# Performance work log

Measured on AMD Instinct MI355X. Metric: run time of the kernel, lower is better.

## Reference

```python
import jax, jax.numpy as jnp
import numpy as np

T, B, H, L = 2048, 32, 512, 2  # seq_len, batch, hidden(=input), num_layers
G = 4 * H
W_SCALE = 0.05  # keep randn-initialized weights out of deep gate saturation


def setup_inputs() -> dict:
    key = jax.random.key(0)
    ks = jax.random.split(key, 5)
    return {
        "x": jax.random.normal(ks[0], (T, B, H), dtype=jnp.float32),
        "w_ih": jax.random.normal(ks[1], (L, G, H), dtype=jnp.float32) * W_SCALE,
        "w_hh": jax.random.normal(ks[2], (L, G, H), dtype=jnp.float32) * W_SCALE,
        "b_ih": jax.random.normal(ks[3], (L, G), dtype=jnp.float32) * W_SCALE,
        "b_hh": jax.random.normal(ks[4], (L, G), dtype=jnp.float32) * W_SCALE,
        "h0": jnp.zeros((L, B, H), dtype=jnp.float32),
        "c0": jnp.zeros((L, B, H), dtype=jnp.float32),
    }


def _lstm_layer(x, w_ih, w_hh, b_ih, b_hh, h0, c0):
    # Precompute input-side gate contributions for all timesteps at once:
    # gates_x[t] = x[t] @ w_ih.T + b_ih + b_hh   (shape [T, B, 4H])
    gates_x = jnp.einsum("tbi,gi->tbg", x, w_ih) + b_ih + b_hh

    def step(carry, gx):
        h, c = carry
        gates = gx + h @ w_hh.T  # [B, 4H]
        i, f, g, o = jnp.split(gates, 4, axis=-1)  # chunk(4, 1) order: i,f,g,o
        i = jax.nn.sigmoid(i)
        f = jax.nn.sigmoid(f)
        g = jnp.tanh(g)
        o = jax.nn.sigmoid(o)
        c = f * c + i * g
        h = o * jnp.tanh(c)
        return (h, c), h

    (hT, cT), ys = jax.lax.scan(step, (h0, c0), gates_x)
    return ys, hT, cT


def reference(x, w_ih, w_hh, b_ih, b_hh, h0, c0):
    out = x
    h_fin, c_fin = [], []
    for l in range(L):  # small fixed stack of structurally identical layers
        out, hT, cT = _lstm_layer(out, w_ih[l], w_hh[l], b_ih[l], b_hh[l], h0[l], c0[l])
        h_fin.append(hT)
        c_fin.append(cT)
    return out, jnp.stack(h_fin), jnp.stack(c_fin)
```

## Files before the change

### kernel.cpp

```cpp
#include <hip/hip_runtime.h>
#include <hip/hip_bf16.h>
#include <stdint.h>

#define T_LEN 2048
#define BATCH 32
#define HID   512
#define GDIM  2048
#define NL    2
#define NBL   32
#define UPB   16
#define RSL   16
#define BH    (BATCH*HID)
#define SLOTB (BH*2)
#define RINGB (RSL*SLOTB)

#define FZ_FB   2048
#define FZ_DET  4096
#define FZ_ABT  4160
#define FZ_TOT  4224

typedef __attribute__((ext_vector_type(8))) __bf16         bf16x8;
typedef __attribute__((ext_vector_type(8))) unsigned short u16x8;
typedef __attribute__((ext_vector_type(4))) unsigned short u16x4;
typedef __attribute__((ext_vector_type(4))) float          f32x4;

__device__ __forceinline__ unsigned short f2bf(float f) {
  unsigned int u = __builtin_bit_cast(unsigned int, f);
  u += 0x7FFFu + ((u >> 16) & 1u);
  return (unsigned short)(u >> 16);
}
__device__ __forceinline__ f32x4 pack8(f32x4 a, f32x4 b) {
  u16x8 r;
  r[0]=f2bf(a[0]); r[1]=f2bf(a[1]); r[2]=f2bf(a[2]); r[3]=f2bf(a[3]);
  r[4]=f2bf(b[0]); r[5]=f2bf(b[1]); r[6]=f2bf(b[2]); r[7]=f2bf(b[3]);
  return __builtin_bit_cast(f32x4, r);
}
__device__ __forceinline__ float sigm(float x)  { return 1.0f / (1.0f + __expf(-x)); }
__device__ __forceinline__ float tanh_(float x) { return 2.0f / (1.0f + __expf(-2.0f*x)) - 1.0f; }

__device__ __forceinline__ f32x4 ld16_pl(const void* p)  { f32x4 r; asm volatile("global_load_dwordx4 %0, %1, off"     : "=v"(r) : "v"(p)); return r; }
__device__ __forceinline__ f32x4 ld16_sc0(const void* p) { f32x4 r; asm volatile("global_load_dwordx4 %0, %1, off sc0" : "=v"(r) : "v"(p)); return r; }
__device__ __forceinline__ f32x4 ld16_sc1(const void* p) { f32x4 r; asm volatile("global_load_dwordx4 %0, %1, off sc1" : "=v"(r) : "v"(p)); return r; }
__device__ __forceinline__ int lddww_sc1(const void* p) {
  int r; asm volatile("global_load_dword %0, %1, off sc1\n\ts_waitcnt vmcnt(0)" : "=v"(r) : "v"(p) : "memory"); return r;
}
__device__ __forceinline__ void st2_sc0(void* p, unsigned short v) {
  unsigned int vv = v; asm volatile("global_store_short %0, %1, off sc0" :: "v"(p), "v"(vv) : "memory");
}
__device__ __forceinline__ void st2_sc1(void* p, unsigned short v) {
  unsigned int vv = v; asm volatile("global_store_short %0, %1, off sc1" :: "v"(p), "v"(vv) : "memory");
}
__device__ __forceinline__ void stdw_sc1(void* p, int v) { asm volatile("global_store_dword %0, %1, off sc1" :: "v"(p), "v"(v) : "memory"); }
__device__ __forceinline__ void vm_drain() { asm volatile("s_waitcnt vmcnt(0)" ::: "memory"); }


__global__ void prep_misc(const float* __restrict__ b_ih, const float* __restrict__ b_hh,
                          const float* __restrict__ h0,
                          int* __restrict__ flagz, float* __restrict__ bsum,
                          char* __restrict__ ring0, char* __restrict__ ring1s) {
  int i = blockIdx.x * blockDim.x + threadIdx.x;
  if (i < FZ_TOT) flagz[i] = 0;
  if (i < NL*GDIM) bsum[i] = b_ih[i] + b_hh[i];
  if (i < NL*2048) {
    int layer = i >> 11, id = i & 2047;
    int mh = id >> 10, ks = (id >> 6) & 15, lf = id & 63;
    int c2 = lf & 15, k2 = lf >> 4;
    const float* s = h0 + ((size_t)(layer*BATCH + mh*16 + c2))*HID + ks*32 + k2*8;
    f32x4 v = pack8(*(const f32x4*)s, *(const f32x4*)(s+4));
    *(f32x4*)(ring0  + (size_t)layer*RINGB + (size_t)id*16) = v;
    *(f32x4*)(ring1s + (size_t)layer*RINGB + (size_t)id*16) = v;
  }
}

__global__ void prep_w(const float* __restrict__ wih, const float* __restrict__ whh,
                       unsigned short* __restrict__ wihb, unsigned short* __restrict__ whhb) {
  const int n4 = NL*GDIM*HID/4;
  for (int i = blockIdx.x*blockDim.x + threadIdx.x; i < 2*n4; i += gridDim.x*blockDim.x) {
    const float*    src = (i < n4) ? wih  : whh;
    unsigned short* dst = (i < n4) ? wihb : whhb;
    int j = (i < n4) ? i : i - n4;
    f32x4 v = *((const f32x4*)src + j);
    u16x4 o; o[0]=f2bf(v[0]); o[1]=f2bf(v[1]); o[2]=f2bf(v[2]); o[3]=f2bf(v[3]);
    *((u16x4*)dst + j) = o;
  }
}


__global__ __launch_bounds__(512, 2) void lstm_persist(
    const float* __restrict__ x, const float* __restrict__ c0,
    const unsigned short* __restrict__ wihb, const unsigned short* __restrict__ whhb,
    const float* __restrict__ bsum,
    char* __restrict__ ring0, char* __restrict__ ring1s,
    int* __restrict__ flagz, float* __restrict__ out) {

  const int bid = blockIdx.x;
  const int r8  = bid & 7;
  if (r8 >= NL) return;
  const int layer = r8;
  const int lb    = bid >> 3;
  const int actIdx = layer*NBL + lb;
  const int tid  = threadIdx.x;
  const int lane = tid & 63;
  const int wave = tid >> 6;
  const int mh = wave & 1, nh = wave >> 1;
  const int col = lane & 15, kg = lane >> 4;
  const int gt  = col & 3;
  const int uu  = nh*4 + (col >> 2);
  const int u0  = lb * UPB;
  const int gu  = u0 + uu;
  const int grow = gt*HID + gu;
  const int tb  = mh*16 + kg*4 + gt;

  int* flagsA = flagz;
  int* flagsB = flagz + FZ_FB;
  int* detect = flagz + FZ_DET;
  int* abortp = flagz + FZ_ABT;

  __shared__ __align__(16) f32x4 smem[4096];

  f32x4 wfx[16], wfh[16];
  {
    const unsigned short* wxr = wihb + ((size_t)(layer*GDIM + grow))*HID + kg*8;
    const unsigned short* whr = whhb + ((size_t)(layer*GDIM + grow))*HID + kg*8;
#pragma unroll
    for (int ks = 0; ks < 16; ++ks) {
      wfx[ks] = *(const f32x4*)(wxr + ks*32);
      wfh[ks] = *(const f32x4*)(whr + ks*32);
    }
  }

  float c = c0[((size_t)layer*BATCH + tb)*HID + gu];
  const float bi  = bsum[layer*GDIM + 0*HID + gu];
  const float bfv = bsum[layer*GDIM + 1*HID + gu];
  const float bg  = bsum[layer*GDIM + 2*HID + gu];
  const float bo  = bsum[layer*GDIM + 3*HID + gu];

  const int se = ((tb>>4)*8192 + (gu>>5)*512 + (tb&15)*8 + ((gu>>3)&3)*128 + (gu&7)) * 2;

  char* ringF = ring0  + (size_t)layer*RINGB;
  char* ringS = ring1s + (size_t)layer*RINGB;
  const char* ringPrev = ring1s;
  int* myfA = flagsA + actIdx*32;
  int* myfB = flagsB + actIdx*32;
  const bool pl = lane < NBL;
  const int* fpOwnA = flagsA + (layer*NBL + lane)*32;
  const int* fpOthB = flagsB + ((1-layer)*NBL + lane)*32;
  int seenOwn = 0, seenOth = 0;
  bool dead = false;

  int xcc = 0;
  asm volatile("s_getreg_b32 %0, hwreg(HW_REG_XCC_ID)" : "=s"(xcc));
  if (tid == 0) stdw_sc1(detect + actIdx, xcc + 1);
  int dv = 0;
  {
    int spins = 0;
    for (;;) {
      if (dv == 0) dv = lddww_sc1(detect + lane);
      if (__all(dv != 0)) break;
      if (((++spins) & 255) == 0) {
        if (lddww_sc1(abortp)) { dead = true; break; }
        if (spins >= (1 << 20)) { stdw_sc1(abortp, 1); dead = true; break; }
      }
    }
  }
  const int dref0 = __shfl(dv, 0, 64), dref1 = __shfl(dv, 32, 64);
  const bool fastL0 = __all((lane < 32) ? (dv != 0 && dv == dref0) : 1);
  const bool fastL1 = __all((lane >= 32) ? (dv != 0 && dv == dref1) : 1);
  const bool fast = (layer ? fastL1 : fastL0) && !dead;

  for (int t = 0; t < T_LEN; ++t) {
    const int slotR = t & (RSL-1);
    const int slotW = (t+1) & (RSL-1);

#pragma unroll
    for (int ks = 0; ks < 16; ++ks)
      asm volatile("" : "+v"(wfx[ks]), "+v"(wfh[ks]));

    f32x4 xpre[8];
    if (layer == 0) {
#pragma unroll
      for (int q = 0; q < 4; ++q) {
        int id = q*512 + tid;
        int mh2 = id >> 10, ks2 = (id >> 6) & 15, lf = id & 63;
        int c2 = lf & 15, k2 = lf >> 4;
        const float* s = x + ((size_t)t*BATCH + mh2*16 + c2)*HID + ks2*32 + k2*8;
        xpre[2*q]   = ld16_pl(s);
        xpre[2*q+1] = ld16_pl(s + 4);
      }
    }

    if (!dead) {
      const int tgt = (layer == 0) ? (t - 14) : (t + 1);
      int spins = 0;
      while (!__all(pl ? (seenOth >= tgt) : 1)) {
        if (pl && seenOth < tgt) { int v = lddww_sc1(fpOthB); if (v > seenOth) seenOth = v; }
        if (((++spins) & 255) == 0) {
          if (lddww_sc1(abortp)) { dead = true; break; }
          if (spins >= (1 << 21)) { stdw_sc1(abortp, 1); dead = true; break; }
        }
      }
    }

    f32x4 xq[4];
    if (layer == 1) {
      const char* p = ringPrev + (size_t)slotW*SLOTB;
#pragma unroll
      for (int q = 0; q < 4; ++q) xq[q] = ld16_sc1(p + (size_t)(q*512 + tid)*16);
    }

    if (!dead) {
      int spins = 0;
      while (!__all(pl ? (seenOwn >= t) : 1)) {
        if (pl && seenOwn < t) { int v = lddww_sc1(fpOwnA); if (v > seenOwn) seenOwn = v; }
        if (((++spins) & 255) == 0) {
          if (lddww_sc1(abortp)) { dead = true; break; }
          if (spins >= (1 << 21)) { stdw_sc1(abortp, 1); dead = true; break; }
        }
      }
    }

    f32x4 hq[4];
    if (fast && t > 0) {
      const char* p = ringF + (size_t)slotR*SLOTB;
#pragma unroll
      for (int q = 0; q < 4; ++q) hq[q] = ld16_sc0(p + (size_t)(q*512 + tid)*16);
    } else {
      const char* p = ringS + (size_t)slotR*SLOTB;
#pragma unroll
      for (int q = 0; q < 4; ++q) hq[q] = ld16_sc1(p + (size_t)(q*512 + tid)*16);
    }
    vm_drain();

#pragma unroll
    for (int q = 0; q < 4; ++q) smem[q*512 + tid] = hq[q];
    if (layer == 0) {
#pragma unroll
      for (int q = 0; q < 4; ++q) smem[2048 + q*512 + tid] = pack8(xpre[2*q], xpre[2*q+1]);
    } else {
#pragma unroll
      for (int q = 0; q < 4; ++q) smem[2048 + q*512 + tid] = xq[q];
    }
    __syncthreads();

    f32x4 accx = {0.f,0.f,0.f,0.f}, acch = {0.f,0.f,0.f,0.f};
    {
      const f32x4* hb = (const f32x4*)smem;
      const f32x4* xb = (const f32x4*)smem + 2048;
#pragma unroll
      for (int ks = 0; ks < 16; ++ks) {
        f32x4 ah = hb[(mh*16 + ks)*64 + lane];
        f32x4 av = xb[(mh*16 + ks)*64 + lane];
        accx = __builtin_amdgcn_mfma_f32_16x16x32_bf16(
                 __builtin_bit_cast(bf16x8, av), __builtin_bit_cast(bf16x8, wfx[ks]), accx, 0,0,0);
        acch = __builtin_amdgcn_mfma_f32_16x16x32_bf16(
                 __builtin_bit_cast(bf16x8, ah), __builtin_bit_cast(bf16x8, wfh[ks]), acch, 0,0,0);
      }
    }
    const f32x4 acc = accx + acch;

    float m0 = acc[0], m1 = acc[1], m2 = acc[2], m3 = acc[3];
    {
      float s0 = __shfl_xor(m0, 1), s1 = __shfl_xor(m1, 1),
            s2 = __shfl_xor(m2, 1), s3 = __shfl_xor(m3, 1);
      if (gt & 1) { m0 = s1; m2 = s3; } else { m1 = s0; m3 = s2; }
      s0 = __shfl_xor(m0, 2); s1 = __shfl_xor(m1, 2);
      s2 = __shfl_xor(m2, 2); s3 = __shfl_xor(m3, 2);
      if (gt & 2) { m0 = s2; m1 = s3; } else { m2 = s0; m3 = s1; }
    }
    const float iv = sigm(m0 + bi), fv = sigm(m1 + bfv);
    const float gv = tanh_(m2 + bg), ov = sigm(m3 + bo);
    c = fv*c + iv*gv;
    const float h = ov * tanh_(c);
    const unsigned short hsh = f2bf(h);

    if (fast) st2_sc0(ringF + (size_t)slotW*SLOTB + se, hsh);
    else      st2_sc1(ringS + (size_t)slotW*SLOTB + se, hsh);
    vm_drain();
    __syncthreads();
    if (tid == 0)  stdw_sc1(myfA, t + 1);
    if (tid == 64) stdw_sc1(myfB, (layer == 0 && fast) ? t : (t + 1));

    if (layer == 0 && fast) st2_sc1(ringS + (size_t)slotW*SLOTB + se, hsh);
    if (layer == 1) out[(size_t)t*BH + (size_t)tb*HID + gu] = h;
    if (t == T_LEN-1) {
      out[(size_t)T_LEN*BH + ((size_t)layer*BATCH + tb)*HID + gu] = h;
      out[(size_t)T_LEN*BH + (size_t)NL*BH + ((size_t)layer*BATCH + tb)*HID + gu] = c;
    }
  }

  vm_drain();
  __syncthreads();
  if (tid == 0)  stdw_sc1(myfA, T_LEN + 1);
  if (tid == 64) stdw_sc1(myfB, T_LEN + 1);
}


extern "C" void kernel_launch(void* const* d_in, const int* in_sizes, int n_in,
                              void* d_out, int out_size, void* d_ws, size_t ws_size,
                              hipStream_t stream) {
  const float* x    = (const float*)d_in[0];
  const float* w_ih = (const float*)d_in[1];
  const float* w_hh = (const float*)d_in[2];
  const float* b_ih = (const float*)d_in[3];
  const float* b_hh = (const float*)d_in[4];
  const float* h0   = (const float*)d_in[5];
  const float* c0   = (const float*)d_in[6];
  float* out = (float*)d_out;

  char* ws = (char*)d_ws;
  size_t off = 0;
  auto alloc = [&](size_t bytes) -> void* {
    off = (off + 255) & ~(size_t)255;
    void* p = ws + off;
    off += bytes;
    return p;
  };
  int*            flagz = (int*)alloc((size_t)FZ_TOT * sizeof(int));
  float*          bsum  = (float*)alloc((size_t)NL*GDIM*sizeof(float));
  char*           ring0 = (char*)alloc((size_t)NL*RINGB);
  char*           ring1s= (char*)alloc((size_t)NL*RINGB);
  unsigned short* wihb  = (unsigned short*)alloc((size_t)NL*GDIM*HID*2);
  unsigned short* whhb  = (unsigned short*)alloc((size_t)NL*GDIM*HID*2);
  (void)ws_size;

  prep_misc<<<64, 256, 0, stream>>>(b_ih, b_hh, h0, flagz, bsum, ring0, ring1s);
  prep_w<<<1024, 256, 0, stream>>>(w_ih, w_hh, wihb, whhb);
  lstm_persist<<<256, 512, 0, stream>>>(x, c0, wihb, whhb, bsum,
                                        ring0, ring1s, flagz, out);
  (void)in_sizes; (void)n_in; (void)out_size;
}
```

Baseline: 8.975 ms.

## Stage h through LDS and publish ring slots with coalesced 16-byte stores

Each block now gathers its bf16 h values in shared memory and one wave writes them to the ring as a single contiguous 1 KB chunk with dwordx4 stores. Before, every thread issued a scattered 2-byte store. The ring layout is reorganised so each block owns a contiguous region, and readers use precomputed offsets. Flag waits are split across waves 0 and 1 followed by a barrier. Layer-1 output rows are written as coalesced float4 stores from LDS, and layer 1 signals its consumer flag earlier. This adds an extra barrier per step and reorders when flags are published relative to the data stores.

```diff
diff --git a/kernel.cpp b/kernel.cpp
--- a/kernel.cpp
+++ b/kernel.cpp
@@ -44,12 +44,8 @@
 __device__ __forceinline__ int lddww_sc1(const void* p) {
   int r; asm volatile("global_load_dword %0, %1, off sc1\n\ts_waitcnt vmcnt(0)" : "=v"(r) : "v"(p) : "memory"); return r;
 }
-__device__ __forceinline__ void st2_sc0(void* p, unsigned short v) {
-  unsigned int vv = v; asm volatile("global_store_short %0, %1, off sc0" :: "v"(p), "v"(vv) : "memory");
-}
-__device__ __forceinline__ void st2_sc1(void* p, unsigned short v) {
-  unsigned int vv = v; asm volatile("global_store_short %0, %1, off sc1" :: "v"(p), "v"(vv) : "memory");
-}
+__device__ __forceinline__ void st16_sc0(void* p, f32x4 v) { asm volatile("global_store_dwordx4 %0, %1, off sc0" :: "v"(p), "v"(v) : "memory"); }
+__device__ __forceinline__ void st16_sc1(void* p, f32x4 v) { asm volatile("global_store_dwordx4 %0, %1, off sc1" :: "v"(p), "v"(v) : "memory"); }
 __device__ __forceinline__ void stdw_sc1(void* p, int v) { asm volatile("global_store_dword %0, %1, off sc1" :: "v"(p), "v"(v) : "memory"); }
 __device__ __forceinline__ void vm_drain() { asm volatile("s_waitcnt vmcnt(0)" ::: "memory"); }
 
@@ -61,14 +57,13 @@
   int i = blockIdx.x * blockDim.x + threadIdx.x;
   if (i < FZ_TOT) flagz[i] = 0;
   if (i < NL*GDIM) bsum[i] = b_ih[i] + b_hh[i];
-  if (i < NL*2048) {
-    int layer = i >> 11, id = i & 2047;
-    int mh = id >> 10, ks = (id >> 6) & 15, lf = id & 63;
-    int c2 = lf & 15, k2 = lf >> 4;
-    const float* s = h0 + ((size_t)(layer*BATCH + mh*16 + c2))*HID + ks*32 + k2*8;
-    f32x4 v = pack8(*(const f32x4*)s, *(const f32x4*)(s+4));
-    *(f32x4*)(ring0  + (size_t)layer*RINGB + (size_t)id*16) = v;
-    *(f32x4*)(ring1s + (size_t)layer*RINGB + (size_t)id*16) = v;
+  if (i < NL*BH) {
+    int layer = i >> 14, e = i & 16383;
+    int b = e >> 9, u = e & 511;
+    unsigned short v = f2bf(h0[((size_t)layer*BATCH + b)*HID + u]);
+    size_t off = (size_t)(u >> 4)*1024 + (size_t)b*32 + (size_t)(u & 15)*2;
+    *(unsigned short*)(ring0  + (size_t)layer*RINGB + off) = v;
+    *(unsigned short*)(ring1s + (size_t)layer*RINGB + off) = v;
   }
 }
 
@@ -117,6 +112,8 @@
   int* abortp = flagz + FZ_ABT;
 
   __shared__ __align__(16) f32x4 smem[4096];
+  __shared__ __align__(16) unsigned short hbuf16[512];
+  __shared__ __align__(16) float houtf[512];
 
   f32x4 wfx[16], wfh[16];
   {
@@ -134,8 +131,6 @@
   const float bfv = bsum[layer*GDIM + 1*HID + gu];
   const float bg  = bsum[layer*GDIM + 2*HID + gu];
   const float bo  = bsum[layer*GDIM + 3*HID + gu];
-
-  const int se = ((tb>>4)*8192 + (gu>>5)*512 + (tb&15)*8 + ((gu>>3)&3)*128 + (gu&7)) * 2;
 
   char* ringF = ring0  + (size_t)layer*RINGB;
   char* ringS = ring1s + (size_t)layer*RINGB;
@@ -168,6 +163,16 @@
   const bool fastL1 = __all((lane >= 32) ? (dv != 0 && dv == dref1) : 1);
   const bool fast = (layer ? fastL1 : fastL0) && !dead;
 
+  int roff[4];
+#pragma unroll
+  for (int q = 0; q < 4; ++q) {
+    int id = q*512 + tid;
+    int mh2 = id >> 10, ks2 = (id >> 6) & 15, lf = id & 63;
+    int ug = ks2*32 + (lf >> 4)*8;
+    int batch = mh2*16 + (lf & 15);
+    roff[q] = (ug >> 4)*1024 + batch*32 + (ug & 8)*2;
+  }
+
   for (int t = 0; t < T_LEN; ++t) {
     const int slotR = t & (RSL-1);
     const int slotW = (t+1) & (RSL-1);
@@ -182,14 +187,23 @@
       for (int q = 0; q < 4; ++q) {
         int id = q*512 + tid;
         int mh2 = id >> 10, ks2 = (id >> 6) & 15, lf = id & 63;
-        int c2 = lf & 15, k2 = lf >> 4;
-        const float* s = x + ((size_t)t*BATCH + mh2*16 + c2)*HID + ks2*32 + k2*8;
+        const float* s = x + ((size_t)t*BATCH + mh2*16 + (lf & 15))*HID + ks2*32 + (lf >> 4)*8;
         xpre[2*q]   = ld16_pl(s);
         xpre[2*q+1] = ld16_pl(s + 4);
       }
     }
 
-    if (!dead) {
+    if (wave == 0 && !dead) {
+      int spins = 0;
+      while (!__all(pl ? (seenOwn >= t) : 1)) {
+        if (pl && seenOwn < t) { int v = lddww_sc1(fpOwnA); if (v > seenOwn) seenOwn = v; }
+        if (((++spins) & 255) == 0) {
+          if (lddww_sc1(abortp)) { dead = true; break; }
+          if (spins >= (1 << 21)) { stdw_sc1(abortp, 1); dead = true; break; }
+        }
+      }
+    }
+    if (wave == 1 && !dead) {
       const int tgt = (layer == 0) ? (t - 14) : (t + 1);
       int spins = 0;
       while (!__all(pl ? (seenOth >= tgt) : 1)) {
@@ -200,34 +214,22 @@
         }
       }
     }
-
-    f32x4 xq[4];
+    __syncthreads();
+
+    f32x4 xq[4], hq[4];
     if (layer == 1) {
       const char* p = ringPrev + (size_t)slotW*SLOTB;
 #pragma unroll
-      for (int q = 0; q < 4; ++q) xq[q] = ld16_sc1(p + (size_t)(q*512 + tid)*16);
-    }
-
-    if (!dead) {
-      int spins = 0;
-      while (!__all(pl ? (seenOwn >= t) : 1)) {
-        if (pl && seenOwn < t) { int v = lddww_sc1(fpOwnA); if (v > seenOwn) seenOwn = v; }
-        if (((++spins) & 255) == 0) {
-          if (lddww_sc1(abortp)) { dead = true; break; }
-          if (spins >= (1 << 21)) { stdw_sc1(abortp, 1); dead = true; break; }
-        }
-      }
-    }
-
-    f32x4 hq[4];
+      for (int q = 0; q < 4; ++q) xq[q] = ld16_sc1(p + roff[q]);
+    }
     if (fast && t > 0) {
       const char* p = ringF + (size_t)slotR*SLOTB;
 #pragma unroll
-      for (int q = 0; q < 4; ++q) hq[q] = ld16_sc0(p + (size_t)(q*512 + tid)*16);
+      for (int q = 0; q < 4; ++q) hq[q] = ld16_sc0(p + roff[q]);
     } else {
       const char* p = ringS + (size_t)slotR*SLOTB;
 #pragma unroll
-      for (int q = 0; q < 4; ++q) hq[q] = ld16_sc1(p + (size_t)(q*512 + tid)*16);
+      for (int q = 0; q < 4; ++q) hq[q] = ld16_sc1(p + roff[q]);
     }
     vm_drain();
 
@@ -241,6 +243,8 @@
       for (int q = 0; q < 4; ++q) smem[2048 + q*512 + tid] = xq[q];
     }
     __syncthreads();
+
+    if (layer == 1 && wave == 1 && lane == 0) stdw_sc1(myfB, t + 1);
 
     f32x4 accx = {0.f,0.f,0.f,0.f}, acch = {0.f,0.f,0.f,0.f};
     {
@@ -271,27 +275,40 @@
     const float gv = tanh_(m2 + bg), ov = sigm(m3 + bo);
     c = fv*c + iv*gv;
     const float h = ov * tanh_(c);
-    const unsigned short hsh = f2bf(h);
-
-    if (fast) st2_sc0(ringF + (size_t)slotW*SLOTB + se, hsh);
-    else      st2_sc1(ringS + (size_t)slotW*SLOTB + se, hsh);
-    vm_drain();
-    __syncthreads();
-    if (tid == 0)  stdw_sc1(myfA, t + 1);
-    if (tid == 64) stdw_sc1(myfB, (layer == 0 && fast) ? t : (t + 1));
-
-    if (layer == 0 && fast) st2_sc1(ringS + (size_t)slotW*SLOTB + se, hsh);
-    if (layer == 1) out[(size_t)t*BH + (size_t)tb*HID + gu] = h;
+
+    hbuf16[tb*16 + uu] = f2bf(h);
+    if (layer == 1) houtf[tb*16 + uu] = h;
     if (t == T_LEN-1) {
       out[(size_t)T_LEN*BH + ((size_t)layer*BATCH + tb)*HID + gu] = h;
       out[(size_t)T_LEN*BH + (size_t)NL*BH + ((size_t)layer*BATCH + tb)*HID + gu] = c;
     }
+    __syncthreads();
+
+    if (wave == 0) {
+      f32x4 v = *(const f32x4*)((const char*)hbuf16 + lane*16);
+      char* d = (fast ? ringF : ringS) + (size_t)slotW*SLOTB + lb*1024 + lane*16;
+      if (fast) st16_sc0(d, v); else st16_sc1(d, v);
+      vm_drain();
+      if (lane == 0) {
+        stdw_sc1(myfA, t + 1);
+        if (layer == 0 && !fast) stdw_sc1(myfB, t + 1);
+      }
+    } else if (wave == 1 && layer == 0 && fast) {
+      f32x4 v = *(const f32x4*)((const char*)hbuf16 + lane*16);
+      st16_sc1(ringS + (size_t)slotW*SLOTB + lb*1024 + lane*16, v);
+      vm_drain();
+      if (lane == 0) stdw_sc1(myfB, t + 1);
+    } else if (layer == 1 && (wave == 2 || wave == 3)) {
+      int l2 = (wave - 2)*64 + lane;
+      int b2 = l2 >> 2, part = l2 & 3;
+      f32x4 v = *(const f32x4*)((const char*)houtf + b2*64 + part*16);
+      *(f32x4*)(out + (size_t)t*BH + (size_t)b2*HID + u0 + part*4) = v;
+    }
   }
 
   vm_drain();
   __syncthreads();
-  if (tid == 0)  stdw_sc1(myfA, T_LEN + 1);
-  if (tid == 64) stdw_sc1(myfB, T_LEN + 1);
+  if (tid == 0) { stdw_sc1(myfA, T_LEN + 1); stdw_sc1(myfB, T_LEN + 1); }
 }
 
 
@@ -323,7 +340,7 @@
   unsigned short* whhb  = (unsigned short*)alloc((size_t)NL*GDIM*HID*2);
   (void)ws_size;
 
-  prep_misc<<<64, 256, 0, stream>>>(b_ih, b_hh, h0, flagz, bsum, ring0, ring1s);
+  prep_misc<<<128, 256, 0, stream>>>(b_ih, b_hh, h0, flagz, bsum, ring0, ring1s);
   prep_w<<<1024, 256, 0, stream>>>(w_ih, w_hh, wihb, whhb);
   lstm_persist<<<256, 512, 0, stream>>>(x, c0, wihb, whhb, bsum,
                                         ring0, ring1s, flagz, out);
```

New measurement: 8.745 ms, median of 2. 2.6% less time.
